# Kernel tuning notes

Hardware: AMD Instinct MI355X
Metric: run time of the kernel (lower is better)

## Reference

```python
import jax, jax.numpy as jnp
import numpy as np

EPS = 1e-6

def _normalize(x, eps=1e-12):
    n = jnp.linalg.norm(x, axis=-1, keepdims=True)
    return x / jnp.maximum(n, eps)

def _gather_nodes(nodes, idx):
    # nodes [B,N,C], idx [B,N,K] -> [B,N,K,C]
    B = nodes.shape[0]
    return nodes[jnp.arange(B)[:, None, None], idx]

def _dist(X, top_k):
    dX = X[:, None, :, :] - X[:, :, None, :]          # [B,N,N,3]
    D = jnp.sqrt(jnp.sum(dX * dX, axis=-1) + EPS)      # [B,N,N]
    neg_vals, E_idx = jax.lax.top_k(-D, top_k)         # smallest distances
    return D, -neg_vals, E_idx

def _gs_dist(D):
    D_min, D_max, D_count = 0.0, 20.0, 15
    D_mu = jnp.linspace(D_min, D_max, D_count)         # [15]
    D_sigma = (D_max - D_min) / D_count
    return jnp.exp(-(((D[..., None] - D_mu) / D_sigma) ** 2))

def _pos_encodings(E_idx, num_embeddings=16):
    N = E_idx.shape[1]
    ii = jnp.arange(N, dtype=jnp.float32)[None, :, None]
    d = (E_idx.astype(jnp.float32) - ii)[..., None]    # [B,N,K,1]
    freq = jnp.exp(jnp.arange(0, num_embeddings, 2, dtype=jnp.float32)
                   * -(np.log(10000.0) / num_embeddings))  # [8]
    angles = d * freq                                   # [B,N,K,8]
    return jnp.concatenate([jnp.cos(angles), jnp.sin(angles)], axis=-1)

def _orientations_coarse(X, E_idx, eps=1e-6):
    dX = X[:, 1:, :] - X[:, :-1, :]
    U = _normalize(dX)
    u_2, u_1, u_0 = U[:, :-2], U[:, 1:-1], U[:, 2:]
    n_2 = _normalize(jnp.cross(u_2, u_1))
    n_1 = _normalize(jnp.cross(u_1, u_0))
    cosA = jnp.clip(-(u_1 * u_0).sum(-1), -1 + eps, 1 - eps)
    A = jnp.arccos(cosA)
    cosD = jnp.clip((n_2 * n_1).sum(-1), -1 + eps, 1 - eps)
    Dang = jnp.sign((u_2 * n_1).sum(-1)) * jnp.arccos(cosD)
    AD = jnp.stack([jnp.cos(A), jnp.sin(A) * jnp.cos(Dang), jnp.sin(A) * jnp.sin(Dang)], axis=2)
    AD = jnp.pad(AD, ((0, 0), (1, 2), (0, 0)))          # [B,N,3]
    o_1 = _normalize(u_2 - u_1)
    O = jnp.stack([o_1, n_2, jnp.cross(o_1, n_2)], axis=2)  # [B,N-3,3,3]
    O = O.reshape(O.shape[0], O.shape[1], 9)
    O = jnp.pad(O, ((0, 0), (1, 2), (0, 0)))            # [B,N,9]
    O_nb = _gather_nodes(O, E_idx)                      # [B,N,K,9]
    X_nb = _gather_nodes(X, E_idx)                      # [B,N,K,3]
    O3 = O.reshape(O.shape[0], O.shape[1], 3, 3)
    dXn = X_nb - X[:, :, None, :]                       # [B,N,K,3]
    dU = jnp.einsum('bnij,bnkj->bnki', O3, dXn)         # rotate into local frame
    dU = _normalize(dU)
    # NOTE: original also computes R = O^T @ O_nb and quaternions Q, but Q is
    # dead code (never returned); omitted here (jit would DCE it anyway).
    return AD, dU

def setup_inputs() -> dict:
    key = jax.random.key(0)
    coords = jax.random.normal(key, (2, 4096, 3), dtype=jnp.float32) * 10.0
    return {"coords": coords, "num_k": 30}

def reference(coords, num_k):
    D, D_neighbors, E_idx = _dist(coords, num_k)
    gs_d = _gs_dist(D_neighbors)
    pos_emb = _pos_encodings(E_idx)
    AD_features, O_features = _orientations_coarse(coords, E_idx)
    return pos_emb, AD_features, O_features, gs_d, D_neighbors, E_idx
```

## Files before the change

### kernel.cpp

```cpp
#include <hip/hip_runtime.h>
#include <hip/hip_bf16.h>

constexpr int B = 2;
constexpr int N = 4096;
constexpr int K = 30;
constexpr int ROWS_PER_BLK = 4;

constexpr size_t OFF_POS = 0;
constexpr size_t OFF_AD  = OFF_POS + (size_t)B * N * K * 16;
constexpr size_t OFF_O   = OFF_AD  + (size_t)B * N * 3;
constexpr size_t OFF_GS  = OFF_O   + (size_t)B * N * K * 3;
constexpr size_t OFF_DN  = OFF_GS  + (size_t)B * N * K * 15;
constexpr size_t OFF_E   = OFF_DN  + (size_t)B * N * K;

constexpr float BIGD = 1e30f;
constexpr unsigned int BIGJ = 0xFFFFFFFFu;

struct F3 { float x, y, z; };

typedef float v2f __attribute__((ext_vector_type(2)));

template <bool ISBF16>
__device__ __forceinline__ float ldx(const void* __restrict__ X, int idx) {
  if constexpr (ISBF16) {
    return __bfloat162float(((const __hip_bfloat16*)X)[idx]);
  } else {
    return ((const float*)X)[idx];
  }
}

template <bool ISBF16>
__device__ __forceinline__ float dist_core(float px, float py, float pz,
                                           float xi, float yi, float zi) {
#pragma clang fp contract(off)
  const float dx = px - xi;
  const float dy = py - yi;
  const float dz = pz - zi;
  return sqrtf(((dx * dx + dy * dy) + dz * dz) + 1e-6f);
}

template <bool ISBF16>
__device__ __forceinline__ float distf(const void* __restrict__ Xb, int j,
                                       float xi, float yi, float zi) {
  float px, py, pz;
  if constexpr (ISBF16) {
    px = ldx<true>(Xb, j * 3 + 0);
    py = ldx<true>(Xb, j * 3 + 1);
    pz = ldx<true>(Xb, j * 3 + 2);
  } else {
    const F3 p = ((const F3*)Xb)[j];
    px = p.x; py = p.y; pz = p.z;
  }
  return dist_core<ISBF16>(px, py, pz, xi, yi, zi);
}

template <int CTRL>
__device__ __forceinline__ float dpp_min_f32(float v) {
  const int mv = __builtin_amdgcn_update_dpp(__float_as_int(BIGD), __float_as_int(v),
                                             CTRL, 0xF, 0xF, false);
  return fminf(__int_as_float(mv), v);
}
template <int CTRL>
__device__ __forceinline__ unsigned int dpp_min_u32(unsigned int v) {
  const unsigned int mv = (unsigned int)__builtin_amdgcn_update_dpp(
      (int)BIGJ, (int)v, CTRL, 0xF, 0xF, false);
  return mv < v ? mv : v;
}
__device__ __forceinline__ float wave_min_f32_bcast(float v) {
  v = dpp_min_f32<0x111>(v);
  v = dpp_min_f32<0x112>(v);
  v = dpp_min_f32<0x114>(v);
  v = dpp_min_f32<0x118>(v);
  v = dpp_min_f32<0x142>(v);
  v = dpp_min_f32<0x143>(v);
  return __int_as_float(__builtin_amdgcn_readlane(__float_as_int(v), 63));
}
__device__ __forceinline__ unsigned int wave_min_u32_bcast(unsigned int v) {
  v = dpp_min_u32<0x111>(v);
  v = dpp_min_u32<0x112>(v);
  v = dpp_min_u32<0x114>(v);
  v = dpp_min_u32<0x118>(v);
  v = dpp_min_u32<0x142>(v);
  v = dpp_min_u32<0x143>(v);
  return (unsigned int)__builtin_amdgcn_readlane((int)v, 63);
}

__device__ __forceinline__ void lex_argmin(float d0, int j0,
                                           float& dmin, unsigned int& jmin) {
  dmin = wave_min_f32_bcast(d0);
  const unsigned long long tie = __ballot(d0 == dmin);
  if (__popcll(tie) == 1) {
    const int wl = __ffsll((unsigned long long)tie) - 1;
    jmin = (unsigned int)__builtin_amdgcn_readlane(j0, wl);
  } else {
    const unsigned int jc = (d0 == dmin) ? (unsigned int)j0 : BIGJ;
    jmin = wave_min_u32_bcast(jc);
  }
}

__device__ __forceinline__ float red2pi(float x) {
  return x - 6.28318530718f * rintf(x * 0.15915494309f);
}

__device__ __forceinline__ void norm3(float& x, float& y, float& z) {
  float n = __builtin_amdgcn_sqrtf((x * x + y * y) + z * z);
  n = fmaxf(n, 1e-12f);
  const float inv = __builtin_amdgcn_rcpf(n);
  x *= inv; y *= inv; z *= inv;
}

__device__ __forceinline__ void cross3(float ax, float ay, float az,
                                       float bx, float by, float bz,
                                       float& cx, float& cy, float& cz) {
  cx = ay * bz - az * by;
  cy = az * bx - ax * bz;
  cz = ax * by - ay * bx;
}

__device__ __forceinline__ void ins2(float d, int j,
                                     float& d0, float& d1, int& j0, int& j1) {
  const bool lt1 = d < d1;
  const float td = lt1 ? d : d1;
  const int   tj = lt1 ? j : j1;
  const bool lt0 = td < d0;
  d1 = lt0 ? d0 : td;  j1 = lt0 ? j0 : tj;
  d0 = lt0 ? td : d0;  j0 = lt0 ? tj : j0;
}

template <bool ISBF16>
__device__ __forceinline__ void body(const void* __restrict__ Xb,
                                     float* __restrict__ out,
                                     int b, int i, int lane) {
  const float xi = ldx<ISBF16>(Xb, i * 3 + 0);
  const float yi = ldx<ISBF16>(Xb, i * 3 + 1);
  const float zi = ldx<ISBF16>(Xb, i * 3 + 2);

  float s0 = BIGD, s1 = BIGD, s2v = BIGD;
  int   j0 = 0x7FFFFFFF, j1 = 0x7FFFFFFF;
  if constexpr (!ISBF16) {
    const F3* __restrict__ P = ((const F3*)Xb) + lane;
    const v2f xyi = {xi, yi};
#pragma unroll 8
    for (int t = 0; t < 64; ++t) {
      const F3 p = P[t * 64];
      const int j = t * 64 + lane;
      float s;
      {
#pragma clang fp contract(off)
        const v2f pxy = {p.x, p.y};
        const v2f a = pxy - xyi;
        const v2f m = a * a;
        const float dz = p.z - zi;
        s = ((m.x + m.y) + dz * dz) + 1e-6f;
      }
      s2v = fminf(fmaxf(s, s1), s2v);
      ins2(s, j, s0, s1, j0, j1);
    }
  } else {
#pragma unroll 8
    for (int t = 0; t < 64; ++t) {
      const int j = t * 64 + lane;
      const float px = ldx<true>(Xb, j * 3 + 0);
      const float py = ldx<true>(Xb, j * 3 + 1);
      const float pz = ldx<true>(Xb, j * 3 + 2);
      float s;
      {
#pragma clang fp contract(off)
        const float dx = px - xi;
        const float dy = py - yi;
        const float dz = pz - zi;
        s = ((dx * dx + dy * dy) + dz * dz) + 1e-6f;
      }
      s2v = fminf(fmaxf(s, s1), s2v);
      ins2(s, j, s0, s1, j0, j1);
    }
  }

  float d0 = sqrtf(s0), d1 = sqrtf(s1);
  {
    const float d2 = sqrtf(s2v);
    if (d0 == d1 && j0 > j1) { const int t = j0; j0 = j1; j1 = t; }
    if (__ballot(d1 == d2) != 0ull) {
      d0 = BIGD; d1 = BIGD; j0 = 0x7FFFFFFF; j1 = 0x7FFFFFFF;
      for (int t = 0; t < 64; ++t) {
        const int j = t * 64 + lane;
        const float d = distf<ISBF16>(Xb, j, xi, yi, zi);
        ins2(d, j, d0, d1, j0, j1);
      }
    }
  }

  unsigned long long exm = 0;
  int   sjv = 0;
  float sdv = 0.0f;
  for (int k = 0; k < K; ++k) {
    float dmin; unsigned int jmin;
    lex_argmin(d0, j0, dmin, jmin);
    if (lane == k) { sjv = (int)jmin; sdv = dmin; }

    const int w  = (int)(jmin & 63u);
    const int tw = (int)(jmin >> 6);
    if (lane == w) {
      exm |= (1ull << tw);
      d0 = d1; j0 = j1;
      d1 = BIGD; j1 = 0x7FFFFFFF;
    }
    if (__ballot(d0 == BIGD) != 0ull) {
      const unsigned int mlo = (unsigned int)__builtin_amdgcn_readlane((int)(unsigned int)(exm & 0xFFFFFFFFull), w);
      const unsigned int mhi = (unsigned int)__builtin_amdgcn_readlane((int)(unsigned int)(exm >> 32), w);
      const unsigned long long m = ((unsigned long long)mhi << 32) | mlo;
      const int j2 = (lane << 6) | w;
      const float d2 = distf<ISBF16>(Xb, j2, xi, yi, zi);
      const float dc = ((m >> lane) & 1ull) ? BIGD : d2;
      float dmin2; unsigned int jmin2;
      lex_argmin(dc, j2, dmin2, jmin2);
      if (lane == w) { d0 = dmin2; j0 = (int)jmin2; }
    }
  }

  float ad0 = 0.f, ad1 = 0.f, ad2 = 0.f;
  float o00 = 0.f, o01 = 0.f, o02 = 0.f;
  float o10 = 0.f, o11 = 0.f, o12 = 0.f;
  float o20 = 0.f, o21 = 0.f, o22 = 0.f;
  if (i >= 1 && i <= N - 3) {
    const float ax = ldx<ISBF16>(Xb, (i - 1) * 3 + 0), ay = ldx<ISBF16>(Xb, (i - 1) * 3 + 1), az = ldx<ISBF16>(Xb, (i - 1) * 3 + 2);
    const float cx = ldx<ISBF16>(Xb, (i + 1) * 3 + 0), cy = ldx<ISBF16>(Xb, (i + 1) * 3 + 1), cz = ldx<ISBF16>(Xb, (i + 1) * 3 + 2);
    const float ex = ldx<ISBF16>(Xb, (i + 2) * 3 + 0), ey = ldx<ISBF16>(Xb, (i + 2) * 3 + 1), ez = ldx<ISBF16>(Xb, (i + 2) * 3 + 2);
    float u2x = xi - ax, u2y = yi - ay, u2z = zi - az; norm3(u2x, u2y, u2z);
    float u1x = cx - xi, u1y = cy - yi, u1z = cz - zi; norm3(u1x, u1y, u1z);
    float u0x = ex - cx, u0y = ey - cy, u0z = ez - cz; norm3(u0x, u0y, u0z);
    float n2x, n2y, n2z; cross3(u2x, u2y, u2z, u1x, u1y, u1z, n2x, n2y, n2z); norm3(n2x, n2y, n2z);
    float n1x, n1y, n1z; cross3(u1x, u1y, u1z, u0x, u0y, u0z, n1x, n1y, n1z); norm3(n1x, n1y, n1z);
    const float dotu = (u1x * u0x + u1y * u0y) + u1z * u0z;
    const float cosA = fminf(fmaxf(-dotu, -1.0f + 1e-6f), 1.0f - 1e-6f);
    const float A = acosf(cosA);
    const float dotn = (n2x * n1x + n2y * n1y) + n2z * n1z;
    const float cosD = fminf(fmaxf(dotn, -1.0f + 1e-6f), 1.0f - 1e-6f);
    const float du2n1 = (u2x * n1x + u2y * n1y) + u2z * n1z;
    const float sg = (du2n1 > 0.f) ? 1.f : ((du2n1 < 0.f) ? -1.f : 0.f);
    const float Dang = sg * acosf(cosD);
    const float sA = __sinf(A),    cA = __cosf(A);
    const float sD = __sinf(Dang), cD = __cosf(Dang);
    ad0 = cA; ad1 = sA * cD; ad2 = sA * sD;
    float o1x = u2x - u1x, o1y = u2y - u1y, o1z = u2z - u1z; norm3(o1x, o1y, o1z);
    o00 = o1x; o01 = o1y; o02 = o1z;
    o10 = n2x; o11 = n2y; o12 = n2z;
    cross3(o1x, o1y, o1z, n2x, n2y, n2z, o20, o21, o22);
  }

  const int row = b * N + i;

  {
    const size_t base = OFF_POS + (size_t)row * (K * 16);
    const int p = lane & 15;
    const float fr = __expf((float)((p & 7) * 2) * -0.57564627f);
    const bool is_cos = (p < 8);
#pragma unroll
    for (int it = 0; it < 8; ++it) {
      const int idx = it * 64 + lane;
      const int k = (idx >> 4) < K ? (idx >> 4) : (K - 1);
      const int jk = __shfl(sjv, k, 64);
      const float df = (float)(jk - i);
      const float r = red2pi(df * fr);
      const float v = is_cos ? __cosf(r) : __sinf(r);
      if (idx < K * 16) out[base + idx] = v;
    }
  }

  {
    const size_t base = OFF_GS + (size_t)row * (K * 15);
#pragma unroll
    for (int it = 0; it < 8; ++it) {
      const int idx = it * 64 + lane;
      const int kq = idx / 15;
      const int k = kq < K ? kq : (K - 1);
      const int m = idx - kq * 15;
      const float d = __shfl(sdv, k, 64);
      const float mu = (float)(m * (20.0 / 14.0));
      const float q = (d - mu) * 0.75f;
      const float v = __expf(-(q * q));
      if (idx < K * 15) out[base + idx] = v;
    }
  }

  if (lane < K) {
    const size_t rowk = (size_t)row * K + lane;
    const int   j = sjv;
    out[OFF_E  + rowk] = (float)j;
    out[OFF_DN + rowk] = sdv;

    float px, py, pz;
    if constexpr (ISBF16) {
      px = ldx<true>(Xb, j * 3 + 0);
      py = ldx<true>(Xb, j * 3 + 1);
      pz = ldx<true>(Xb, j * 3 + 2);
    } else {
      const F3 p = ((const F3*)Xb)[j];
      px = p.x; py = p.y; pz = p.z;
    }
    const float gx = px - xi, gy = py - yi, gz = pz - zi;
    const float v0 = (o00 * gx + o01 * gy) + o02 * gz;
    const float v1 = (o10 * gx + o11 * gy) + o12 * gz;
    const float v2 = (o20 * gx + o21 * gy) + o22 * gz;
    const float nn = fmaxf(__builtin_amdgcn_sqrtf((v0 * v0 + v1 * v1) + v2 * v2), 1e-12f);
    const float inv = __builtin_amdgcn_rcpf(nn);
    out[OFF_O + rowk * 3 + 0] = v0 * inv;
    out[OFF_O + rowk * 3 + 1] = v1 * inv;
    out[OFF_O + rowk * 3 + 2] = v2 * inv;
  } else if (lane < K + 3) {
    const int c = lane - K;
    const float v = (c == 0) ? ad0 : (c == 1) ? ad1 : ad2;
    out[OFF_AD + (size_t)row * 3 + c] = v;
  }
}

__global__ __launch_bounds__(64 * ROWS_PER_BLK)
void protein_feat_kernel(const void* __restrict__ X,
                         float* __restrict__ out) {
  const int lane = threadIdx.x & 63;
  const int wv   = threadIdx.x >> 6;
  const int row  = blockIdx.x * ROWS_PER_BLK + wv;
  const int b    = row >> 12;
  const int i    = row & (N - 1);

  const unsigned short h = ((const unsigned short*)X)[2 * lane];
  const int e = (h >> 7) & 0xFF;
  const bool sane = ((h & 0x7FFF) == 0) || (e >= 115 && e <= 134);
  const unsigned long long bal = __ballot(sane);
  const bool isbf16 = __popcll(bal) >= 40;

  if (isbf16) {
    const void* Xb = (const void*)((const __hip_bfloat16*)X + (size_t)b * N * 3);
    body<true>(Xb, out, b, i, lane);
  } else {
    const void* Xb = (const void*)((const float*)X + (size_t)b * N * 3);
    body<false>(Xb, out, b, i, lane);
  }
}

extern "C" void kernel_launch(void* const* d_in, const int* in_sizes, int n_in,
                              void* d_out, int out_size, void* d_ws, size_t ws_size,
                              hipStream_t stream) {
  const void* X = d_in[0];
  float* out = (float*)d_out;
  (void)in_sizes; (void)n_in; (void)d_ws; (void)ws_size; (void)out_size;
  protein_feat_kernel<<<dim3(B * N / ROWS_PER_BLK), dim3(64 * ROWS_PER_BLK), 0, stream>>>(X, out);
}
```

Measured before the change: 107.9 us.

## Use med3-based top-3 scan with split streams, uniform readlane check, closed-form angles

Replaces the per-lane top-2/third-smallest scan with an fmed3-based insertion step and splits the 64-point scan into two independent interleaved streams that are merged afterwards, which shortens the dependency chain and cuts per-step instructions. The refill check in the K-selection loop now reads a single lane instead of running a wave-wide ballot. The acos/sin/cos chain for the dihedral features is replaced with sqrt(1-c^2) identities. This adds merge logic with tie-handling risk and small numerical differences in the angle features.

```diff
diff --git a/kernel.cpp b/kernel.cpp
--- a/kernel.cpp
+++ b/kernel.cpp
@@ -127,6 +127,19 @@
   d0 = lt0 ? td : d0;  j0 = lt0 ? tj : j0;
 }
 
+__device__ __forceinline__ void step_med3(float s, int T,
+                                          float& s0, float& s1, float& s2,
+                                          int& t0, int& t1) {
+  const bool c0 = s < s0;
+  const bool c1 = s < s1;
+  const float n2 = __builtin_amdgcn_fmed3f(s, s1, s2);
+  const float n1 = __builtin_amdgcn_fmed3f(s, s0, s1);
+  const float n0 = fminf(s, s0);
+  t1 = c0 ? t0 : (c1 ? T : t1);
+  t0 = c0 ? T : t0;
+  s2 = n2; s1 = n1; s0 = n0;
+}
+
 template <bool ISBF16>
 __device__ __forceinline__ void body(const void* __restrict__ Xb,
                                      float* __restrict__ out,
@@ -135,58 +148,106 @@
   const float yi = ldx<ISBF16>(Xb, i * 3 + 1);
   const float zi = ldx<ISBF16>(Xb, i * 3 + 2);
 
-  float s0 = BIGD, s1 = BIGD, s2v = BIGD;
-  int   j0 = 0x7FFFFFFF, j1 = 0x7FFFFFFF;
-  if constexpr (!ISBF16) {
-    const F3* __restrict__ P = ((const F3*)Xb) + lane;
-    const v2f xyi = {xi, yi};
+  float d0, d1;
+  int   j0, j1;
+  bool  hazard;
+  {
+    float s0m, s1m, s2m;
+    int   t0m, t1m;
+    if constexpr (!ISBF16) {
+      const F3* __restrict__ P = ((const F3*)Xb) + lane;
+      const v2f xyi = {xi, yi};
+      float sA0 = BIGD, sA1 = BIGD, sA2 = BIGD;
+      float sB0 = BIGD, sB1 = BIGD, sB2 = BIGD;
+      int tA0 = 0, tA1 = 0, tB0 = 32, tB1 = 32;
+#pragma unroll
+      for (int tt = 0; tt < 32; ++tt) {
+        {
+          const F3 p = P[tt * 64];
+          float s;
+          {
+#pragma clang fp contract(off)
+            const v2f pxy = {p.x, p.y};
+            const v2f a = pxy - xyi;
+            const v2f m = a * a;
+            const float dz = p.z - zi;
+            s = ((m.x + m.y) + dz * dz) + 1e-6f;
+          }
+          step_med3(s, tt, sA0, sA1, sA2, tA0, tA1);
+        }
+        {
+          const F3 p = P[(tt + 32) * 64];
+          float s;
+          {
+#pragma clang fp contract(off)
+            const v2f pxy = {p.x, p.y};
+            const v2f a = pxy - xyi;
+            const v2f m = a * a;
+            const float dz = p.z - zi;
+            s = ((m.x + m.y) + dz * dz) + 1e-6f;
+          }
+          step_med3(s, tt + 32, sB0, sB1, sB2, tB0, tB1);
+        }
+      }
+      const bool bfirst = sB0 < sA0;
+      s0m = bfirst ? sB0 : sA0;
+      t0m = bfirst ? tB0 : tA0;
+      const float sx = bfirst ? sA0 : sB0;
+      const int   tx = bfirst ? tA0 : tB0;
+      const bool bsec = sB1 < sA1;
+      const float sy = bsec ? sB1 : sA1;
+      const int   ty = bsec ? tB1 : tA1;
+      const bool pickY = (sy < sx) || (sy == sx && ty < tx);
+      s1m = pickY ? sy : sx;
+      t1m = pickY ? ty : tx;
+      const float xm = fmaxf(sA0, sB0);
+      const float ym = fminf(sA1, sB1);
+      const float t3 = fmaxf(xm, ym);
+      const float z  = fminf(fmaxf(sA1, sB1), fminf(sA2, sB2));
+      s2m = fminf(t3, z);
+      j0 = (t0m << 6) | lane;
+      j1 = (t1m << 6) | lane;
+    } else {
+      float s0 = BIGD, s1 = BIGD, s2 = BIGD;
+      int jj0 = 0x7FFFFFFF, jj1 = 0x7FFFFFFF;
 #pragma unroll 8
-    for (int t = 0; t < 64; ++t) {
-      const F3 p = P[t * 64];
-      const int j = t * 64 + lane;
-      float s;
-      {
+      for (int t = 0; t < 64; ++t) {
+        const int j = t * 64 + lane;
+        const float px = ldx<true>(Xb, j * 3 + 0);
+        const float py = ldx<true>(Xb, j * 3 + 1);
+        const float pz = ldx<true>(Xb, j * 3 + 2);
+        float s;
+        {
 #pragma clang fp contract(off)
-        const v2f pxy = {p.x, p.y};
-        const v2f a = pxy - xyi;
-        const v2f m = a * a;
-        const float dz = p.z - zi;
-        s = ((m.x + m.y) + dz * dz) + 1e-6f;
+          const float dx = px - xi;
+          const float dy = py - yi;
+          const float dz = pz - zi;
+          s = ((dx * dx + dy * dy) + dz * dz) + 1e-6f;
+        }
+        const bool c0 = s < s0;
+        const bool c1 = s < s1;
+        const float n2 = __builtin_amdgcn_fmed3f(s, s1, s2);
+        const float n1 = __builtin_amdgcn_fmed3f(s, s0, s1);
+        const float n0 = fminf(s, s0);
+        jj1 = c0 ? jj0 : (c1 ? j : jj1);
+        jj0 = c0 ? j : jj0;
+        s2 = n2; s1 = n1; s0 = n0;
       }
-      s2v = fminf(fmaxf(s, s1), s2v);
-      ins2(s, j, s0, s1, j0, j1);
-    }
-  } else {
-#pragma unroll 8
+      s0m = s0; s1m = s1; s2m = s2; j0 = jj0; j1 = jj1;
+      t0m = 0; t1m = 0; (void)t0m; (void)t1m;
+    }
+
+    d0 = sqrtf(s0m); d1 = sqrtf(s1m);
+    const float d2v = sqrtf(s2m);
+    if (d0 == d1 && j0 > j1) { const int t = j0; j0 = j1; j1 = t; }
+    hazard = (__ballot(d1 == d2v) != 0ull);
+  }
+  if (hazard) {
+    d0 = BIGD; d1 = BIGD; j0 = 0x7FFFFFFF; j1 = 0x7FFFFFFF;
     for (int t = 0; t < 64; ++t) {
       const int j = t * 64 + lane;
-      const float px = ldx<true>(Xb, j * 3 + 0);
-      const float py = ldx<true>(Xb, j * 3 + 1);
-      const float pz = ldx<true>(Xb, j * 3 + 2);
-      float s;
-      {
-#pragma clang fp contract(off)
-        const float dx = px - xi;
-        const float dy = py - yi;
-        const float dz = pz - zi;
-        s = ((dx * dx + dy * dy) + dz * dz) + 1e-6f;
-      }
-      s2v = fminf(fmaxf(s, s1), s2v);
-      ins2(s, j, s0, s1, j0, j1);
-    }
-  }
-
-  float d0 = sqrtf(s0), d1 = sqrtf(s1);
-  {
-    const float d2 = sqrtf(s2v);
-    if (d0 == d1 && j0 > j1) { const int t = j0; j0 = j1; j1 = t; }
-    if (__ballot(d1 == d2) != 0ull) {
-      d0 = BIGD; d1 = BIGD; j0 = 0x7FFFFFFF; j1 = 0x7FFFFFFF;
-      for (int t = 0; t < 64; ++t) {
-        const int j = t * 64 + lane;
-        const float d = distf<ISBF16>(Xb, j, xi, yi, zi);
-        ins2(d, j, d0, d1, j0, j1);
-      }
+      const float d = distf<ISBF16>(Xb, j, xi, yi, zi);
+      ins2(d, j, d0, d1, j0, j1);
     }
   }
 
@@ -205,7 +266,7 @@
       d0 = d1; j0 = j1;
       d1 = BIGD; j1 = 0x7FFFFFFF;
     }
-    if (__ballot(d0 == BIGD) != 0ull) {
+    if (__builtin_amdgcn_readlane(__float_as_int(d0), w) == __float_as_int(BIGD)) {
       const unsigned int mlo = (unsigned int)__builtin_amdgcn_readlane((int)(unsigned int)(exm & 0xFFFFFFFFull), w);
       const unsigned int mhi = (unsigned int)__builtin_amdgcn_readlane((int)(unsigned int)(exm >> 32), w);
       const unsigned long long m = ((unsigned long long)mhi << 32) | mlo;
@@ -233,15 +294,13 @@
     float n1x, n1y, n1z; cross3(u1x, u1y, u1z, u0x, u0y, u0z, n1x, n1y, n1z); norm3(n1x, n1y, n1z);
     const float dotu = (u1x * u0x + u1y * u0y) + u1z * u0z;
     const float cosA = fminf(fmaxf(-dotu, -1.0f + 1e-6f), 1.0f - 1e-6f);
-    const float A = acosf(cosA);
+    const float sinA = __builtin_amdgcn_sqrtf(fmaxf(1.0f - cosA * cosA, 0.0f));
     const float dotn = (n2x * n1x + n2y * n1y) + n2z * n1z;
     const float cosD = fminf(fmaxf(dotn, -1.0f + 1e-6f), 1.0f - 1e-6f);
+    const float sinDm = __builtin_amdgcn_sqrtf(fmaxf(1.0f - cosD * cosD, 0.0f));
     const float du2n1 = (u2x * n1x + u2y * n1y) + u2z * n1z;
     const float sg = (du2n1 > 0.f) ? 1.f : ((du2n1 < 0.f) ? -1.f : 0.f);
-    const float Dang = sg * acosf(cosD);
-    const float sA = __sinf(A),    cA = __cosf(A);
-    const float sD = __sinf(Dang), cD = __cosf(Dang);
-    ad0 = cA; ad1 = sA * cD; ad2 = sA * sD;
+    ad0 = cosA; ad1 = sinA * cosD; ad2 = sinA * (sg * sinDm);
     float o1x = u2x - u1x, o1y = u2y - u1y, o1z = u2z - u1z; norm3(o1x, o1y, o1z);
     o00 = o1x; o01 = o1y; o02 = o1z;
     o10 = n2x; o11 = n2y; o12 = n2z;
```

After: 145.8 us. 1.35x slower.
